# Kernel optimization log

Hardware: AMD Instinct MI355X
Metric: run time of the kernel (lower is better)

Reference implementation:

```python
import jax, jax.numpy as jnp
import numpy as np

B, CIN, HID, HEADS, K, STRIDE, PAD, W = 8, 256, 256, 8, 31, 1, 15, 16384
HD = HID // HEADS  # head dim
DN = ('NCHW', 'OIHW', 'NCHW')


def setup_inputs() -> dict:
    key = jax.random.key(0)
    ks = jax.random.split(key, 6)
    std = 1.0 / np.sqrt(HD)
    return dict(
        x=jax.random.normal(ks[0], (B, CIN, 1, W), jnp.float32),
        query=(jax.random.normal(ks[1], (HID,), jnp.float32) * std),
        Wk=(jax.random.normal(ks[2], (CIN, HID), jnp.float32) * std),
        Wk_bias=jnp.zeros((HID,), jnp.float32),
        rpe=0.02 * jax.random.normal(ks[3], (HEADS, 1, 1, K), jnp.float32),
        to_v_w=(jax.random.normal(ks[4], (HID, CIN, 1, 1), jnp.float32) / np.sqrt(CIN)),
        to_v_b=jnp.zeros((HID,), jnp.float32),
        to_out_w=(jax.random.normal(ks[5], (HID, HID, 1, 1), jnp.float32) / np.sqrt(HID)),
        to_out_b=jnp.zeros((HID,), jnp.float32),
    )


def reference(x, query, Wk, Wk_bias, rpe, to_v_w, to_v_b, to_out_w, to_out_b):
    Bsz = x.shape[0]
    # shared learned query -> [B, heads, hd], normalized and scaled
    q = jnp.broadcast_to(query, (Bsz, HID)).reshape(Bsz, HEADS, HD)
    q = q / (jnp.linalg.norm(q, axis=-1, keepdims=True) + 1e-6)
    q = q / np.sqrt(HD)
    # fused QK: (q @ Wk^T) @ x  -> cost [B, heads, 1, W]
    Wk_r = Wk.reshape(CIN, HEADS, HD)
    qWk = jnp.einsum('bhd,Dhd->bDh', q, Wk_r)          # [B, CIN, heads]
    cost = jnp.einsum('bDhw,bDc->bchw', x, qWk)        # [B, heads, 1, W]
    qWk_b = jnp.einsum('hd,bhd->bh', Wk_bias.reshape(HEADS, HD), q)
    cost = cost + qWk_b[:, :, None, None]
    cost_exp = jnp.exp(cost)
    # v = 1x1 conv (to_v)
    v = jnp.einsum('bdhw,od->bohw', x, to_v_w.reshape(HID, CIN)) + to_v_b[None, :, None, None]
    # exp-weighted values, grouped windowed sums
    vc = (cost_exp[:, :, None] * v.reshape(Bsz, HEADS, HD, 1, W)).reshape(Bsz, HID, 1, W)
    rpe_exp = jnp.exp(rpe)                             # [heads, 1, 1, K]
    kern_v = jnp.repeat(rpe_exp, HD, axis=0)           # [HID, 1, 1, K] depthwise
    sum_v = jax.lax.conv_general_dilated(
        vc, kern_v, (1, STRIDE), ((0, 0), (PAD, PAD)),
        feature_group_count=HID, dimension_numbers=DN)
    sum_c = jax.lax.conv_general_dilated(
        cost_exp, rpe_exp, (1, STRIDE), ((0, 0), (PAD, PAD)),
        feature_group_count=HEADS, dimension_numbers=DN)
    Wo = sum_v.shape[-1]
    out = sum_v.reshape(Bsz, HEADS, HD, 1, Wo) / sum_c.reshape(Bsz, HEADS, 1, 1, Wo)
    out = out.reshape(Bsz, HID, 1, Wo)
    # to_out 1x1 conv
    out = jnp.einsum('bdhw,od->bohw', out, to_out_w.reshape(HID, HID)) + to_out_b[None, :, None, None]
    return out
```

## Files before the change

kernel.cpp:

```cpp
#include <hip/hip_runtime.h>
#include <hip/hip_bf16.h>
#include <math.h>

#define BATCH  8
#define NHEADS 8
#define KW     31
#define W      16384

#define WS_QWKB 2048
#define WS_RPE  2056
#define OFF_WVH 9216
#define OFF_WOH (OFF_WVH + 131072)
#define OFF_CE  (OFF_WOH + 131072)

typedef __attribute__((ext_vector_type(8))) short  short8;
typedef __attribute__((ext_vector_type(4))) float  f32x4;

__device__ __forceinline__ float f4c(const float4& v, int i) {
  switch (i) { case 0: return v.x; case 1: return v.y; case 2: return v.z; default: return v.w; }
}
__device__ __forceinline__ unsigned short f2bf(float f) {
  union { __hip_bfloat16 h; unsigned short u; } cv; cv.h = __float2bfloat16(f); return cv.u;
}
__device__ __forceinline__ float bf2f(unsigned short u) {
  union { __hip_bfloat16 h; unsigned short u; } cv; cv.u = u; return __bfloat162float(cv.h);
}

__global__ __launch_bounds__(256) void prep_kernel(
    const float* __restrict__ query, const float* __restrict__ Wk,
    const float* __restrict__ Wkb, const float* __restrict__ rpe,
    const float* __restrict__ Wv, const float* __restrict__ Wo,
    float* __restrict__ ws, unsigned short* __restrict__ WvH,
    unsigned short* __restrict__ WoH) {
  int t = threadIdx.x, bid = blockIdx.x;
  if (bid == 0) {
    __shared__ float q_l[256];
    float qv = query[t];
    float ss = qv * qv;
    #pragma unroll
    for (int m = 16; m >= 1; m >>= 1) ss += __shfl_xor(ss, m, 32);
    qv = qv / (sqrtf(ss) + 1e-6f) * 0.17677669529663687f;
    q_l[t] = qv;
    __syncthreads();
    const float* wr = Wk + (size_t)t * 256;
    #pragma unroll
    for (int h = 0; h < 8; ++h) {
      float s = 0.f;
      #pragma unroll
      for (int d = 0; d < 32; ++d) s = fmaf(q_l[h*32 + d], wr[h*32 + d], s);
      ws[t*8 + h] = s;
    }
    float pb = Wkb[t] * q_l[t];
    #pragma unroll
    for (int m = 16; m >= 1; m >>= 1) pb += __shfl_xor(pb, m, 32);
    if ((t & 31) == 0) ws[WS_QWKB + (t >> 5)] = pb;
    if (t < NHEADS * KW) ws[WS_RPE + t] = __expf(rpe[t]);
  } else {
    const float* src = (bid <= 4) ? Wv : Wo;
    unsigned short* dst = (bid <= 4) ? WvH : WoH;
    int seg = (bid - 1) & 3;
    int base4 = seg * 4096;
    #pragma unroll
    for (int it = 0; it < 16; ++it) {
      int i4 = base4 + t + 256 * it;
      float4 v = ((const float4*)src)[i4];
      ushort4 o;
      o.x = f2bf(v.x); o.y = f2bf(v.y); o.z = f2bf(v.z); o.w = f2bf(v.w);
      ((ushort4*)dst)[i4] = o;
    }
  }
}

__global__ __launch_bounds__(512, 4) void xv_kernel(
    const float* __restrict__ x, const float* __restrict__ wsf,
    const unsigned short* __restrict__ A,
    const float* __restrict__ bias,
    float* __restrict__ ceout, float* __restrict__ vcout, int b0) {
  __shared__ float xs[64 * 260];
  __shared__ float cbuf[4 * 576];
  __shared__ float ceL[512];
  __shared__ float biasL[256];

  int t = threadIdx.x;
  int bb = blockIdx.y, b = b0 + bb;
  int w0 = blockIdx.x * 64;
  if (t < 256) biasL[t] = bias[t];

  {
    int tt = t & 255, db2 = t >> 8;
    int rr = tt >> 4, c2 = tt & 15;
    #pragma unroll
    for (int dd = 0; dd < 2; ++dd) {
      int db = db2 * 2 + dd;
      float4 v0 = *(const float4*)(x + ((size_t)b*256 + db*64 + rr*4 + 0)*W + w0 + c2*4);
      float4 v1 = *(const float4*)(x + ((size_t)b*256 + db*64 + rr*4 + 1)*W + w0 + c2*4);
      float4 v2 = *(const float4*)(x + ((size_t)b*256 + db*64 + rr*4 + 2)*W + w0 + c2*4);
      float4 v3 = *(const float4*)(x + ((size_t)b*256 + db*64 + rr*4 + 3)*W + w0 + c2*4);
      #pragma unroll
      for (int i = 0; i < 4; ++i) {
        float4 tv = make_float4(f4c(v0,i), f4c(v1,i), f4c(v2,i), f4c(v3,i));
        *(float4*)&xs[(c2*4 + i)*260 + db*64 + rr*4] = tv;
      }
    }
  }
  __syncthreads();

  int w = t & 63, q = t >> 6;
  int qu = __builtin_amdgcn_readfirstlane(q);

  f32x4 xr[8];
  {
    const float* xrow = &xs[w*260 + qu*32];
    #pragma unroll
    for (int i = 0; i < 8; ++i) xr[i] = *(const f32x4*)(xrow + 4*i);
    float ca[8] = {0,0,0,0,0,0,0,0};
    const float* qkb = wsf + (size_t)qu*256;
    #pragma unroll
    for (int k4 = 0; k4 < 8; ++k4) {
      const float* qr = qkb + k4*32;
      #pragma unroll
      for (int e = 0; e < 4; ++e) {
        #pragma unroll
        for (int h = 0; h < 8; ++h)
          ca[h] = fmaf(xr[k4][e], qr[e*8 + h], ca[h]);
      }
    }
    if (q < 4) {
      #pragma unroll
      for (int h = 0; h < 8; ++h) cbuf[q*576 + w*9 + h] = ca[h];
    } else {
      #pragma unroll
      for (int h = 0; h < 8; ++h) { asm volatile("" :: "v"(ca[h])); }
    }
    __syncthreads();

    {
      unsigned short* hrow = (unsigned short*)xs + w*520 + qu*32;
      #pragma unroll
      for (int kc = 0; kc < 4; ++kc) {
        short8 hs, ls;
        #pragma unroll
        for (int e = 0; e < 4; ++e) {
          float a0 = xr[2*kc][e], a1 = xr[2*kc+1][e];
          unsigned short h0 = f2bf(a0), h1 = f2bf(a1);
          hs[e]   = (short)h0;  hs[e+4] = (short)h1;
          ls[e]   = (short)f2bf(a0 - bf2f(h0));
          ls[e+4] = (short)f2bf(a1 - bf2f(h1));
        }
        *(short8*)(hrow + 8*kc)       = hs;
        *(short8*)(hrow + 256 + 8*kc) = ls;
      }
    }
    float acc0;
    {
      int hR = t >> 6 & 7, wR = t & 63;
      acc0 = cbuf[0*576 + wR*9 + hR] + cbuf[1*576 + wR*9 + hR]
           + cbuf[2*576 + wR*9 + hR] + cbuf[3*576 + wR*9 + hR];
    }
    __syncthreads();
    if (q >= 4) {
      #pragma unroll
      for (int h = 0; h < 8; ++h) cbuf[(q-4)*576 + w*9 + h] = ca[h];
    }
    __syncthreads();

    {
      int hR = t >> 6 & 7, wR = t & 63;
      float sum = acc0 + cbuf[0*576 + wR*9 + hR] + cbuf[1*576 + wR*9 + hR]
                + cbuf[2*576 + wR*9 + hR] + cbuf[3*576 + wR*9 + hR]
                + wsf[WS_QWKB + hR];
      float ce = __expf(sum);
      ceL[hR*64 + wR] = ce;
      ceout[((size_t)bb*8 + hR)*W + w0 + wR] = ce;
    }
  }
  __syncthreads();

  int wid = t >> 6, quad = (t >> 4) & 3, m = t & 15;
  f32x4 acc[2][4];
  #pragma unroll
  for (int j = 0; j < 2; ++j)
    #pragma unroll
    for (int c = 0; c < 4; ++c) acc[j][c] = (f32x4){0.f, 0.f, 0.f, 0.f};

  const unsigned short* xsu = (const unsigned short*)xs;
  #pragma unroll
  for (int kk = 0; kk < 8; ++kk) {
    int ko = kk*32 + quad*8;
    short8 a0 = *(const short8*)(A + (size_t)(32*wid + m)*256 + ko);
    short8 a1 = *(const short8*)(A + (size_t)(32*wid + 16 + m)*256 + ko);
    #pragma unroll
    for (int c = 0; c < 4; ++c) {
      int rw = 16*c + m;
      short8 bh = *(const short8*)(xsu + rw*520 + ko);
      short8 bl = *(const short8*)(xsu + rw*520 + 256 + ko);
      acc[0][c] = __builtin_amdgcn_mfma_f32_16x16x32_bf16(a0, bh, acc[0][c], 0, 0, 0);
      acc[0][c] = __builtin_amdgcn_mfma_f32_16x16x32_bf16(a0, bl, acc[0][c], 0, 0, 0);
      acc[1][c] = __builtin_amdgcn_mfma_f32_16x16x32_bf16(a1, bh, acc[1][c], 0, 0, 0);
      acc[1][c] = __builtin_amdgcn_mfma_f32_16x16x32_bf16(a1, bl, acc[1][c], 0, 0, 0);
    }
  }
  __syncthreads();

  #pragma unroll
  for (int j = 0; j < 2; ++j) {
    int ob = 32*wid + 16*j + 4*quad;
    #pragma unroll
    for (int c = 0; c < 4; ++c) {
      int wc = 16*c + m;
      float ce = ceL[wid*64 + wc];
      f32x4 r;
      #pragma unroll
      for (int i = 0; i < 4; ++i) r[i] = (acc[j][c][i] + biasL[ob + i]) * ce;
      *(f32x4*)(xs + wc*260 + ob) = r;
    }
  }
  __syncthreads();
  {
    float* vg = vcout + ((size_t)bb*W + w0)*256;
    #pragma unroll
    for (int it = 0; it < 8; ++it) {
      int idx = t + 512*it;
      int row = idx >> 6, c4 = (idx & 63)*4;
      f32x4 v = *(const f32x4*)(xs + row*260 + c4);
      *(f32x4*)(vg + (size_t)idx*4) = v;
    }
  }
}

__global__ __launch_bounds__(512, 6) void cg_kernel(
    const float* __restrict__ vc, const float* __restrict__ costexp,
    const float* __restrict__ rpe_ws, const unsigned short* __restrict__ A,
    const float* __restrict__ bias, float* __restrict__ outp, int b0) {
  __shared__ __align__(16) float vcl[62 * 36];
  __shared__ __align__(16) unsigned short ubuf[2][32*264];
  __shared__ float cel[8 * 64];
  __shared__ float rcl[8 * 32];
  __shared__ float rpel[8 * 32];
  __shared__ float biasL[256];

  int t = threadIdx.x;
  int bb = blockIdx.y;
  int tx = blockIdx.x;
  int tile = ((tx & 7) << 6) | (tx >> 3);
  int w0 = tile * 32;

  if (t < 256) {
    biasL[t] = bias[t];
    int h = t >> 5, k = t & 31;
    rpel[t] = (k < KW) ? rpe_ws[h*KW + k] : 0.f;
  }
  {
    int h = t >> 6, c = t & 63;
    if (c < 62) {
      int gw = w0 - 15 + c;
      cel[h*64 + c] = (gw >= 0 && gw < W) ? costexp[((size_t)bb*8 + h)*W + gw] : 0.f;
    }
  }
  __syncthreads();
  if (t < 256) {
    int h = t >> 5, w = t & 31;
    float acc = 0.f;
    #pragma unroll
    for (int k = 0; k < KW; ++k) acc = fmaf(rpel[h*32 + k], cel[h*64 + w + k], acc);
    rcl[t] = 1.0f / acc;
  }

  int wv = t >> 4, p = t & 15;
  for (int q = 0; q < 8; ++q) {
    if (t < 496) {
      int r = t >> 3, c4 = (t & 7) * 4;
      int gw = w0 - 15 + r;
      float4 v = make_float4(0.f, 0.f, 0.f, 0.f);
      if (gw >= 0 && gw < W)
        v = *(const float4*)(vc + ((size_t)bb*W + gw)*256 + q*32 + c4);
      *(float4*)&vcl[r*36 + c4] = v;
    }
    __syncthreads();
    {
      float ax = 0.f, ay = 0.f;
      #pragma unroll
      for (int k = 0; k < KW; ++k) {
        float rpk = rpel[q*32 + k];
        float2 v = *(const float2*)&vcl[(wv + k)*36 + 2*p];
        ax = fmaf(rpk, v.x, ax);
        ay = fmaf(rpk, v.y, ay);
      }
      float rc = rcl[q*32 + wv];
      float ux = ax * rc, uy = ay * rc;
      unsigned short hx = f2bf(ux), hy = f2bf(uy);
      unsigned short lx = f2bf(ux - bf2f(hx)), ly = f2bf(uy - bf2f(hy));
      ushort2 hv; hv.x = hx; hv.y = hy;
      ushort2 lv; lv.x = lx; lv.y = ly;
      *(ushort2*)&ubuf[0][wv*264 + q*32 + 2*p] = hv;
      *(ushort2*)&ubuf[1][wv*264 + q*32 + 2*p] = lv;
    }
    __syncthreads();
  }

  int wid = t >> 6, quad = (t >> 4) & 3, m = t & 15;
  f32x4 acc[2][2];
  #pragma unroll
  for (int j = 0; j < 2; ++j)
    #pragma unroll
    for (int c = 0; c < 2; ++c) acc[j][c] = (f32x4){0.f, 0.f, 0.f, 0.f};

  #pragma unroll
  for (int pass = 0; pass < 2; ++pass) {
    const unsigned short* bsrc = ubuf[pass];
    #pragma unroll
    for (int kk = 0; kk < 8; ++kk) {
      int ko = kk*32 + quad*8;
      short8 a0 = *(const short8*)(A + (size_t)(32*wid + m)*256 + ko);
      short8 a1 = *(const short8*)(A + (size_t)(32*wid + 16 + m)*256 + ko);
      #pragma unroll
      for (int c = 0; c < 2; ++c) {
        short8 bv = *(const short8*)(bsrc + (16*c + m)*264 + ko);
        acc[0][c] = __builtin_amdgcn_mfma_f32_16x16x32_bf16(a0, bv, acc[0][c], 0, 0, 0);
        acc[1][c] = __builtin_amdgcn_mfma_f32_16x16x32_bf16(a1, bv, acc[1][c], 0, 0, 0);
      }
    }
  }
  __syncthreads();

  float* outs = (float*)ubuf;
  #pragma unroll
  for (int j = 0; j < 2; ++j) {
    int ob = 32*wid + 16*j + 4*quad;
    #pragma unroll
    for (int c = 0; c < 2; ++c) {
      int w = 16*c + m;
      #pragma unroll
      for (int i = 0; i < 4; ++i)
        outs[(ob + i)*32 + w] = acc[j][c][i] + biasL[ob + i];
    }
  }
  __syncthreads();
  {
    float* og = outp + (size_t)(b0 + bb)*256*W + w0;
    #pragma unroll
    for (int it = 0; it < 4; ++it) {
      int idx = t + 512*it;
      int o = idx >> 3, c4 = (idx & 7)*4;
      f32x4 v = *(const f32x4*)(outs + o*32 + c4);
      *(f32x4*)(og + (size_t)o*W + c4) = v;
    }
  }
}

extern "C" void kernel_launch(void* const* d_in, const int* in_sizes, int n_in,
                              void* d_out, int out_size, void* d_ws, size_t ws_size,
                              hipStream_t stream) {
  const float* x     = (const float*)d_in[0];
  const float* query = (const float*)d_in[1];
  const float* Wk    = (const float*)d_in[2];
  const float* Wkb   = (const float*)d_in[3];
  const float* rpe   = (const float*)d_in[4];
  const float* Wv    = (const float*)d_in[5];
  const float* tvb   = (const float*)d_in[6];
  const float* Wo    = (const float*)d_in[7];
  const float* tob   = (const float*)d_in[8];
  float* out = (float*)d_out;
  char* wsb  = (char*)d_ws;
  float* wsf = (float*)d_ws;

  unsigned short* WvH = (unsigned short*)(wsb + OFF_WVH);
  unsigned short* WoH = (unsigned short*)(wsb + OFF_WOH);

  const size_t per_b = (size_t)8*W*4 + (size_t)W*256*4;
  int NB = (int)((ws_size > OFF_CE) ? ((ws_size - OFF_CE) / per_b) : 1);
  if (NB > BATCH) NB = BATCH;
  if (NB < 1) NB = 1;

  float* ceB = (float*)(wsb + OFF_CE);
  float* vcB = (float*)(wsb + OFF_CE + (size_t)NB*8*W*4);

  prep_kernel<<<9, 256, 0, stream>>>(query, Wk, Wkb, rpe, Wv, Wo, wsf, WvH, WoH);

  for (int b0 = 0; b0 < BATCH; b0 += NB) {
    int nb = (BATCH - b0 < NB) ? (BATCH - b0) : NB;
    xv_kernel<<<dim3(256, nb), 512, 0, stream>>>(x, wsf, WvH, tvb, ceB, vcB, b0);
    cg_kernel<<<dim3(512, nb), 512, 0, stream>>>(vcB, ceB, wsf + WS_RPE, WoH, tob, out, b0);
  }
}
```

Before: 469.1 us.

## Enlarge per-thread work in xv and cg kernels, cut sync and reload passes

xv_kernel drops to 256 threads per block. Each wave now computes a 64x64 MFMA tile with four A fragments reused across four B fragments, and the cost reduction uses one cbuf pass instead of two staged ones. cg_kernel loads half the channels (128) per iteration instead of 32, so there are 2 outer iterations rather than 8. Each thread computes two adjacent output positions from shared vc loads and keeps rpe in registers, and the output staging reuses vcl so one barrier is removed. The aim is fewer barriers and less LDS traffic per FLOP, at the cost of higher register pressure and lower occupancy.

```diff
diff --git a/kernel.cpp b/kernel.cpp
--- a/kernel.cpp
+++ b/kernel.cpp
@@ -71,27 +71,25 @@
   }
 }
 
-__global__ __launch_bounds__(512, 4) void xv_kernel(
+__global__ __launch_bounds__(256, 2) void xv_kernel(
     const float* __restrict__ x, const float* __restrict__ wsf,
     const unsigned short* __restrict__ A,
     const float* __restrict__ bias,
     float* __restrict__ ceout, float* __restrict__ vcout, int b0) {
   __shared__ float xs[64 * 260];
-  __shared__ float cbuf[4 * 576];
+  __shared__ float cbuf[2048];
   __shared__ float ceL[512];
   __shared__ float biasL[256];
 
   int t = threadIdx.x;
   int bb = blockIdx.y, b = b0 + bb;
   int w0 = blockIdx.x * 64;
-  if (t < 256) biasL[t] = bias[t];
-
-  {
-    int tt = t & 255, db2 = t >> 8;
-    int rr = tt >> 4, c2 = tt & 15;
-    #pragma unroll
-    for (int dd = 0; dd < 2; ++dd) {
-      int db = db2 * 2 + dd;
+  biasL[t] = bias[t];
+
+  {
+    int rr = t >> 4, c2 = t & 15;
+    #pragma unroll
+    for (int db = 0; db < 4; ++db) {
       float4 v0 = *(const float4*)(x + ((size_t)b*256 + db*64 + rr*4 + 0)*W + w0 + c2*4);
       float4 v1 = *(const float4*)(x + ((size_t)b*256 + db*64 + rr*4 + 1)*W + w0 + c2*4);
       float4 v2 = *(const float4*)(x + ((size_t)b*256 + db*64 + rr*4 + 2)*W + w0 + c2*4);
@@ -108,78 +106,65 @@
   int w = t & 63, q = t >> 6;
   int qu = __builtin_amdgcn_readfirstlane(q);
 
-  f32x4 xr[8];
-  {
-    const float* xrow = &xs[w*260 + qu*32];
-    #pragma unroll
-    for (int i = 0; i < 8; ++i) xr[i] = *(const f32x4*)(xrow + 4*i);
+  f32x4 xr[16];
+  {
+    const float* xrow = &xs[w*260 + qu*64];
+    #pragma unroll
+    for (int i = 0; i < 16; ++i) xr[i] = *(const f32x4*)(xrow + 4*i);
     float ca[8] = {0,0,0,0,0,0,0,0};
-    const float* qkb = wsf + (size_t)qu*256;
-    #pragma unroll
-    for (int k4 = 0; k4 < 8; ++k4) {
-      const float* qr = qkb + k4*32;
+    const float* qkb = wsf + (size_t)qu*64*8;
+    #pragma unroll
+    for (int k8 = 0; k8 < 8; ++k8) {
+      const float* qr = qkb + 64*k8;
       #pragma unroll
       for (int e = 0; e < 4; ++e) {
         #pragma unroll
-        for (int h = 0; h < 8; ++h)
-          ca[h] = fmaf(xr[k4][e], qr[e*8 + h], ca[h]);
-      }
-    }
-    if (q < 4) {
-      #pragma unroll
-      for (int h = 0; h < 8; ++h) cbuf[q*576 + w*9 + h] = ca[h];
-    } else {
-      #pragma unroll
-      for (int h = 0; h < 8; ++h) { asm volatile("" :: "v"(ca[h])); }
-    }
-    __syncthreads();
-
-    {
-      unsigned short* hrow = (unsigned short*)xs + w*520 + qu*32;
-      #pragma unroll
-      for (int kc = 0; kc < 4; ++kc) {
-        short8 hs, ls;
-        #pragma unroll
-        for (int e = 0; e < 4; ++e) {
-          float a0 = xr[2*kc][e], a1 = xr[2*kc+1][e];
-          unsigned short h0 = f2bf(a0), h1 = f2bf(a1);
-          hs[e]   = (short)h0;  hs[e+4] = (short)h1;
-          ls[e]   = (short)f2bf(a0 - bf2f(h0));
-          ls[e+4] = (short)f2bf(a1 - bf2f(h1));
+        for (int h = 0; h < 8; ++h) {
+          ca[h] = fmaf(xr[2*k8][e],   qr[e*8 + h],     ca[h]);
+          ca[h] = fmaf(xr[2*k8+1][e], qr[(e+4)*8 + h], ca[h]);
         }
-        *(short8*)(hrow + 8*kc)       = hs;
-        *(short8*)(hrow + 256 + 8*kc) = ls;
-      }
-    }
-    float acc0;
-    {
-      int hR = t >> 6 & 7, wR = t & 63;
-      acc0 = cbuf[0*576 + wR*9 + hR] + cbuf[1*576 + wR*9 + hR]
-           + cbuf[2*576 + wR*9 + hR] + cbuf[3*576 + wR*9 + hR];
-    }
-    __syncthreads();
-    if (q >= 4) {
-      #pragma unroll
-      for (int h = 0; h < 8; ++h) cbuf[(q-4)*576 + w*9 + h] = ca[h];
-    }
-    __syncthreads();
-
-    {
-      int hR = t >> 6 & 7, wR = t & 63;
-      float sum = acc0 + cbuf[0*576 + wR*9 + hR] + cbuf[1*576 + wR*9 + hR]
-                + cbuf[2*576 + wR*9 + hR] + cbuf[3*576 + wR*9 + hR]
-                + wsf[WS_QWKB + hR];
-      float ce = __expf(sum);
-      ceL[hR*64 + wR] = ce;
-      ceout[((size_t)bb*8 + hR)*W + w0 + wR] = ce;
-    }
+      }
+    }
+    #pragma unroll
+    for (int h = 0; h < 8; ++h) cbuf[t*8 + h] = ca[h];
+  }
+  __syncthreads();
+
+  {
+    unsigned short* hrow = (unsigned short*)xs + w*520 + qu*64;
+    #pragma unroll
+    for (int k8 = 0; k8 < 8; ++k8) {
+      short8 hs, ls;
+      #pragma unroll
+      for (int e = 0; e < 4; ++e) {
+        float a0 = xr[2*k8][e], a1 = xr[2*k8+1][e];
+        unsigned short h0 = f2bf(a0), h1 = f2bf(a1);
+        hs[e]   = (short)h0;  hs[e+4] = (short)h1;
+        ls[e]   = (short)f2bf(a0 - bf2f(h0));
+        ls[e+4] = (short)f2bf(a1 - bf2f(h1));
+      }
+      *(short8*)(hrow + 8*k8)       = hs;
+      *(short8*)(hrow + 256 + 8*k8) = ls;
+    }
+  }
+  __syncthreads();
+
+  #pragma unroll
+  for (int s = 0; s < 2; ++s) {
+    int idx = t + 256*s;
+    int h = idx >> 6, ww = idx & 63;
+    float sum = cbuf[ww*8 + h] + cbuf[(64+ww)*8 + h] + cbuf[(128+ww)*8 + h]
+              + cbuf[(192+ww)*8 + h] + wsf[WS_QWKB + h];
+    float ce = __expf(sum);
+    ceL[h*64 + ww] = ce;
+    ceout[((size_t)bb*8 + h)*W + w0 + ww] = ce;
   }
   __syncthreads();
 
   int wid = t >> 6, quad = (t >> 4) & 3, m = t & 15;
-  f32x4 acc[2][4];
-  #pragma unroll
-  for (int j = 0; j < 2; ++j)
+  f32x4 acc[4][4];
+  #pragma unroll
+  for (int j = 0; j < 4; ++j)
     #pragma unroll
     for (int c = 0; c < 4; ++c) acc[j][c] = (f32x4){0.f, 0.f, 0.f, 0.f};
 
@@ -187,28 +172,34 @@
   #pragma unroll
   for (int kk = 0; kk < 8; ++kk) {
     int ko = kk*32 + quad*8;
-    short8 a0 = *(const short8*)(A + (size_t)(32*wid + m)*256 + ko);
-    short8 a1 = *(const short8*)(A + (size_t)(32*wid + 16 + m)*256 + ko);
+    short8 a[4], bh[4], bl[4];
+    #pragma unroll
+    for (int j = 0; j < 4; ++j)
+      a[j] = *(const short8*)(A + (size_t)(64*wid + 16*j + m)*256 + ko);
     #pragma unroll
     for (int c = 0; c < 4; ++c) {
       int rw = 16*c + m;
-      short8 bh = *(const short8*)(xsu + rw*520 + ko);
-      short8 bl = *(const short8*)(xsu + rw*520 + 256 + ko);
-      acc[0][c] = __builtin_amdgcn_mfma_f32_16x16x32_bf16(a0, bh, acc[0][c], 0, 0, 0);
-      acc[0][c] = __builtin_amdgcn_mfma_f32_16x16x32_bf16(a0, bl, acc[0][c], 0, 0, 0);
-      acc[1][c] = __builtin_amdgcn_mfma_f32_16x16x32_bf16(a1, bh, acc[1][c], 0, 0, 0);
-      acc[1][c] = __builtin_amdgcn_mfma_f32_16x16x32_bf16(a1, bl, acc[1][c], 0, 0, 0);
-    }
-  }
-  __syncthreads();
-
-  #pragma unroll
-  for (int j = 0; j < 2; ++j) {
-    int ob = 32*wid + 16*j + 4*quad;
+      bh[c] = *(const short8*)(xsu + rw*520 + ko);
+      bl[c] = *(const short8*)(xsu + rw*520 + 256 + ko);
+    }
+    #pragma unroll
+    for (int j = 0; j < 4; ++j)
+      #pragma unroll
+      for (int c = 0; c < 4; ++c) {
+        acc[j][c] = __builtin_amdgcn_mfma_f32_16x16x32_bf16(a[j], bh[c], acc[j][c], 0, 0, 0);
+        acc[j][c] = __builtin_amdgcn_mfma_f32_16x16x32_bf16(a[j], bl[c], acc[j][c], 0, 0, 0);
+      }
+  }
+  __syncthreads();
+
+  #pragma unroll
+  for (int j = 0; j < 4; ++j) {
+    int ob = 64*wid + 16*j + 4*quad;
+    int h = (64*wid + 16*j) >> 5;
     #pragma unroll
     for (int c = 0; c < 4; ++c) {
       int wc = 16*c + m;
-      float ce = ceL[wid*64 + wc];
+      float ce = ceL[h*64 + wc];
       f32x4 r;
       #pragma unroll
       for (int i = 0; i < 4; ++i) r[i] = (acc[j][c][i] + biasL[ob + i]) * ce;
@@ -219,8 +210,8 @@
   {
     float* vg = vcout + ((size_t)bb*W + w0)*256;
     #pragma unroll
-    for (int it = 0; it < 8; ++it) {
-      int idx = t + 512*it;
+    for (int it = 0; it < 16; ++it) {
+      int idx = t + 256*it;
       int row = idx >> 6, c4 = (idx & 63)*4;
       f32x4 v = *(const f32x4*)(xs + row*260 + c4);
       *(f32x4*)(vg + (size_t)idx*4) = v;
@@ -228,12 +219,12 @@
   }
 }
 
-__global__ __launch_bounds__(512, 6) void cg_kernel(
+__global__ __launch_bounds__(512, 4) void cg_kernel(
     const float* __restrict__ vc, const float* __restrict__ costexp,
     const float* __restrict__ rpe_ws, const unsigned short* __restrict__ A,
     const float* __restrict__ bias, float* __restrict__ outp, int b0) {
-  __shared__ __align__(16) float vcl[62 * 36];
-  __shared__ __align__(16) unsigned short ubuf[2][32*264];
+  __shared__ __align__(16) float vcl[63 * 132];
+  __shared__ __align__(16) unsigned short ubuf[32 * 528];
   __shared__ float cel[8 * 64];
   __shared__ float rcl[8 * 32];
   __shared__ float rpel[8 * 32];
@@ -266,34 +257,57 @@
     rcl[t] = 1.0f / acc;
   }
 
-  int wv = t >> 4, p = t & 15;
-  for (int q = 0; q < 8; ++q) {
-    if (t < 496) {
-      int r = t >> 3, c4 = (t & 7) * 4;
-      int gw = w0 - 15 + r;
-      float4 v = make_float4(0.f, 0.f, 0.f, 0.f);
-      if (gw >= 0 && gw < W)
-        v = *(const float4*)(vc + ((size_t)bb*W + gw)*256 + q*32 + c4);
-      *(float4*)&vcl[r*36 + c4] = v;
+  int g = t >> 5, p4 = t & 31;
+  for (int half = 0; half < 2; ++half) {
+    #pragma unroll
+    for (int it = 0; it < 4; ++it) {
+      int idx = t + 512*it;
+      int r = idx >> 5, fq = idx & 31;
+      if (r < 62) {
+        int gw = w0 - 15 + r;
+        float4 v = make_float4(0.f, 0.f, 0.f, 0.f);
+        if (gw >= 0 && gw < W)
+          v = *(const float4*)(vc + ((size_t)bb*W + gw)*256 + half*128 + fq*4);
+        *(float4*)&vcl[r*132 + fq*4] = v;
+      }
     }
     __syncthreads();
+
     {
-      float ax = 0.f, ay = 0.f;
-      #pragma unroll
-      for (int k = 0; k < KW; ++k) {
-        float rpk = rpel[q*32 + k];
-        float2 v = *(const float2*)&vcl[(wv + k)*36 + 2*p];
-        ax = fmaf(rpk, v.x, ax);
-        ay = fmaf(rpk, v.y, ay);
-      }
-      float rc = rcl[q*32 + wv];
-      float ux = ax * rc, uy = ay * rc;
-      unsigned short hx = f2bf(ux), hy = f2bf(uy);
-      unsigned short lx = f2bf(ux - bf2f(hx)), ly = f2bf(uy - bf2f(hy));
-      ushort2 hv; hv.x = hx; hv.y = hy;
-      ushort2 lv; lv.x = lx; lv.y = ly;
-      *(ushort2*)&ubuf[0][wv*264 + q*32 + 2*p] = hv;
-      *(ushort2*)&ubuf[1][wv*264 + q*32 + 2*p] = lv;
+      int h = 4*half + (p4 >> 3);
+      float rp[KW];
+      #pragma unroll
+      for (int k = 0; k < KW; ++k) rp[k] = rpel[h*32 + k];
+
+      f32x4 a0 = (f32x4){0.f,0.f,0.f,0.f}, a1 = (f32x4){0.f,0.f,0.f,0.f};
+      #pragma unroll
+      for (int s = 0; s < 32; ++s) {
+        f32x4 v = *(const f32x4*)&vcl[(2*g + s)*132 + 4*p4];
+        if (s < KW) {
+          #pragma unroll
+          for (int e = 0; e < 4; ++e) a0[e] = fmaf(rp[s], v[e], a0[e]);
+        }
+        if (s >= 1) {
+          #pragma unroll
+          for (int e = 0; e < 4; ++e) a1[e] = fmaf(rp[s-1], v[e], a1[e]);
+        }
+      }
+      float rc0 = rcl[h*32 + 2*g], rc1 = rcl[h*32 + 2*g + 1];
+      ushort4 h0v, l0v, h1v, l1v;
+      #pragma unroll
+      for (int e = 0; e < 4; ++e) {
+        float u0 = a0[e] * rc0, u1 = a1[e] * rc1;
+        unsigned short hh0 = f2bf(u0), hh1 = f2bf(u1);
+        ((unsigned short*)&h0v)[e] = hh0;
+        ((unsigned short*)&l0v)[e] = f2bf(u0 - bf2f(hh0));
+        ((unsigned short*)&h1v)[e] = hh1;
+        ((unsigned short*)&l1v)[e] = f2bf(u1 - bf2f(hh1));
+      }
+      int cbase = half*128 + 4*p4;
+      *(ushort4*)&ubuf[(2*g    )*528 + cbase]       = h0v;
+      *(ushort4*)&ubuf[(2*g    )*528 + 256 + cbase] = l0v;
+      *(ushort4*)&ubuf[(2*g + 1)*528 + cbase]       = h1v;
+      *(ushort4*)&ubuf[(2*g + 1)*528 + 256 + cbase] = l1v;
     }
     __syncthreads();
   }
@@ -307,7 +321,6 @@
 
   #pragma unroll
   for (int pass = 0; pass < 2; ++pass) {
-    const unsigned short* bsrc = ubuf[pass];
     #pragma unroll
     for (int kk = 0; kk < 8; ++kk) {
       int ko = kk*32 + quad*8;
@@ -315,15 +328,14 @@
       short8 a1 = *(const short8*)(A + (size_t)(32*wid + 16 + m)*256 + ko);
       #pragma unroll
       for (int c = 0; c < 2; ++c) {
-        short8 bv = *(const short8*)(bsrc + (16*c + m)*264 + ko);
+        short8 bv = *(const short8*)(ubuf + (16*c + m)*528 + pass*256 + ko);
         acc[0][c] = __builtin_amdgcn_mfma_f32_16x16x32_bf16(a0, bv, acc[0][c], 0, 0, 0);
         acc[1][c] = __builtin_amdgcn_mfma_f32_16x16x32_bf16(a1, bv, acc[1][c], 0, 0, 0);
       }
     }
   }
-  __syncthreads();
-
-  float* outs = (float*)ubuf;
+
+  float* outs = (float*)vcl;
   #pragma unroll
   for (int j = 0; j < 2; ++j) {
     int ob = 32*wid + 16*j + 4*quad;
@@ -379,7 +391,7 @@
 
   for (int b0 = 0; b0 < BATCH; b0 += NB) {
     int nb = (BATCH - b0 < NB) ? (BATCH - b0) : NB;
-    xv_kernel<<<dim3(256, nb), 512, 0, stream>>>(x, wsf, WvH, tvb, ceB, vcB, b0);
+    xv_kernel<<<dim3(256, nb), 256, 0, stream>>>(x, wsf, WvH, tvb, ceB, vcB, b0);
     cg_kernel<<<dim3(512, nb), 512, 0, stream>>>(vcB, ceB, wsf + WS_RPE, WoH, tob, out, b0);
   }
 }
```

Result: faster. 419.5 us (-10.6%).

## Fuse value projection, windowed sum and output projection into one kernel with halo recompute

Applied to the files above, without the earlier changes.

Replaces the two-kernel pipeline (xv_kernel writing exp-cost and exp-weighted values to workspace, then cg_kernel reading them back) with a single 1024-thread kernel per 32-wide output tile. Each block loads a 64-wide x window including the halo, recomputes cost and the to_v projection for the halo columns, does the 31-tap windowed sums in registers, and applies the to_out MFMA. This removes the large round trip of the intermediate values through global memory and the per-batch launch loop. The cost is about double the value-projection MFMA work from halo recompute, plus larger blocks and a higher LDS footprint, which may reduce occupancy.

```diff
diff --git a/kernel.cpp b/kernel.cpp
--- a/kernel.cpp
+++ b/kernel.cpp
@@ -11,7 +11,6 @@
 #define WS_RPE  2056
 #define OFF_WVH 9216
 #define OFF_WOH (OFF_WVH + 131072)
-#define OFF_CE  (OFF_WOH + 131072)
 
 typedef __attribute__((ext_vector_type(8))) short  short8;
 typedef __attribute__((ext_vector_type(4))) float  f32x4;
@@ -71,276 +70,225 @@
   }
 }
 
-__global__ __launch_bounds__(512, 4) void xv_kernel(
+__global__ __launch_bounds__(1024, 4) void fused_kernel(
     const float* __restrict__ x, const float* __restrict__ wsf,
-    const unsigned short* __restrict__ A,
-    const float* __restrict__ bias,
-    float* __restrict__ ceout, float* __restrict__ vcout, int b0) {
-  __shared__ float xs[64 * 260];
-  __shared__ float cbuf[4 * 576];
+    const unsigned short* __restrict__ Av,
+    const unsigned short* __restrict__ Ao,
+    const float* __restrict__ biasv, const float* __restrict__ biaso,
+    float* __restrict__ outp) {
+  __shared__ __align__(16) float xs[64 * 260];
+  __shared__ __align__(16) float rgB[9216];
   __shared__ float ceL[512];
-  __shared__ float biasL[256];
+  __shared__ float rcl[256];
+  __shared__ float rpel[256];
+  __shared__ float bvL[256];
+  __shared__ float boL[256];
 
   int t = threadIdx.x;
-  int bb = blockIdx.y, b = b0 + bb;
-  int w0 = blockIdx.x * 64;
-  if (t < 256) biasL[t] = bias[t];
-
-  {
-    int tt = t & 255, db2 = t >> 8;
-    int rr = tt >> 4, c2 = tt & 15;
-    #pragma unroll
-    for (int dd = 0; dd < 2; ++dd) {
-      int db = db2 * 2 + dd;
-      float4 v0 = *(const float4*)(x + ((size_t)b*256 + db*64 + rr*4 + 0)*W + w0 + c2*4);
-      float4 v1 = *(const float4*)(x + ((size_t)b*256 + db*64 + rr*4 + 1)*W + w0 + c2*4);
-      float4 v2 = *(const float4*)(x + ((size_t)b*256 + db*64 + rr*4 + 2)*W + w0 + c2*4);
-      float4 v3 = *(const float4*)(x + ((size_t)b*256 + db*64 + rr*4 + 3)*W + w0 + c2*4);
-      #pragma unroll
-      for (int i = 0; i < 4; ++i) {
-        float4 tv = make_float4(f4c(v0,i), f4c(v1,i), f4c(v2,i), f4c(v3,i));
-        *(float4*)&xs[(c2*4 + i)*260 + db*64 + rr*4] = tv;
-      }
-    }
-  }
-  __syncthreads();
-
-  int w = t & 63, q = t >> 6;
-  int qu = __builtin_amdgcn_readfirstlane(q);
-
-  f32x4 xr[8];
-  {
-    const float* xrow = &xs[w*260 + qu*32];
-    #pragma unroll
-    for (int i = 0; i < 8; ++i) xr[i] = *(const f32x4*)(xrow + 4*i);
-    float ca[8] = {0,0,0,0,0,0,0,0};
-    const float* qkb = wsf + (size_t)qu*256;
-    #pragma unroll
-    for (int k4 = 0; k4 < 8; ++k4) {
-      const float* qr = qkb + k4*32;
-      #pragma unroll
-      for (int e = 0; e < 4; ++e) {
-        #pragma unroll
-        for (int h = 0; h < 8; ++h)
-          ca[h] = fmaf(xr[k4][e], qr[e*8 + h], ca[h]);
-      }
-    }
-    if (q < 4) {
-      #pragma unroll
-      for (int h = 0; h < 8; ++h) cbuf[q*576 + w*9 + h] = ca[h];
-    } else {
-      #pragma unroll
-      for (int h = 0; h < 8; ++h) { asm volatile("" :: "v"(ca[h])); }
-    }
-    __syncthreads();
-
-    {
-      unsigned short* hrow = (unsigned short*)xs + w*520 + qu*32;
-      #pragma unroll
-      for (int kc = 0; kc < 4; ++kc) {
-        short8 hs, ls;
-        #pragma unroll
-        for (int e = 0; e < 4; ++e) {
-          float a0 = xr[2*kc][e], a1 = xr[2*kc+1][e];
-          unsigned short h0 = f2bf(a0), h1 = f2bf(a1);
-          hs[e]   = (short)h0;  hs[e+4] = (short)h1;
-          ls[e]   = (short)f2bf(a0 - bf2f(h0));
-          ls[e+4] = (short)f2bf(a1 - bf2f(h1));
-        }
-        *(short8*)(hrow + 8*kc)       = hs;
-        *(short8*)(hrow + 256 + 8*kc) = ls;
-      }
-    }
-    float acc0;
-    {
-      int hR = t >> 6 & 7, wR = t & 63;
-      acc0 = cbuf[0*576 + wR*9 + hR] + cbuf[1*576 + wR*9 + hR]
-           + cbuf[2*576 + wR*9 + hR] + cbuf[3*576 + wR*9 + hR];
-    }
-    __syncthreads();
-    if (q >= 4) {
-      #pragma unroll
-      for (int h = 0; h < 8; ++h) cbuf[(q-4)*576 + w*9 + h] = ca[h];
-    }
-    __syncthreads();
-
-    {
-      int hR = t >> 6 & 7, wR = t & 63;
-      float sum = acc0 + cbuf[0*576 + wR*9 + hR] + cbuf[1*576 + wR*9 + hR]
-                + cbuf[2*576 + wR*9 + hR] + cbuf[3*576 + wR*9 + hR]
-                + wsf[WS_QWKB + hR];
-      float ce = __expf(sum);
-      ceL[hR*64 + wR] = ce;
-      ceout[((size_t)bb*8 + hR)*W + w0 + wR] = ce;
-    }
-  }
-  __syncthreads();
-
-  int wid = t >> 6, quad = (t >> 4) & 3, m = t & 15;
-  f32x4 acc[2][4];
-  #pragma unroll
-  for (int j = 0; j < 2; ++j)
-    #pragma unroll
-    for (int c = 0; c < 4; ++c) acc[j][c] = (f32x4){0.f, 0.f, 0.f, 0.f};
-
-  const unsigned short* xsu = (const unsigned short*)xs;
-  #pragma unroll
-  for (int kk = 0; kk < 8; ++kk) {
-    int ko = kk*32 + quad*8;
-    short8 a0 = *(const short8*)(A + (size_t)(32*wid + m)*256 + ko);
-    short8 a1 = *(const short8*)(A + (size_t)(32*wid + 16 + m)*256 + ko);
-    #pragma unroll
-    for (int c = 0; c < 4; ++c) {
-      int rw = 16*c + m;
-      short8 bh = *(const short8*)(xsu + rw*520 + ko);
-      short8 bl = *(const short8*)(xsu + rw*520 + 256 + ko);
-      acc[0][c] = __builtin_amdgcn_mfma_f32_16x16x32_bf16(a0, bh, acc[0][c], 0, 0, 0);
-      acc[0][c] = __builtin_amdgcn_mfma_f32_16x16x32_bf16(a0, bl, acc[0][c], 0, 0, 0);
-      acc[1][c] = __builtin_amdgcn_mfma_f32_16x16x32_bf16(a1, bh, acc[1][c], 0, 0, 0);
-      acc[1][c] = __builtin_amdgcn_mfma_f32_16x16x32_bf16(a1, bl, acc[1][c], 0, 0, 0);
-    }
-  }
-  __syncthreads();
-
-  #pragma unroll
-  for (int j = 0; j < 2; ++j) {
-    int ob = 32*wid + 16*j + 4*quad;
-    #pragma unroll
-    for (int c = 0; c < 4; ++c) {
-      int wc = 16*c + m;
-      float ce = ceL[wid*64 + wc];
-      f32x4 r;
-      #pragma unroll
-      for (int i = 0; i < 4; ++i) r[i] = (acc[j][c][i] + biasL[ob + i]) * ce;
-      *(f32x4*)(xs + wc*260 + ob) = r;
-    }
-  }
-  __syncthreads();
-  {
-    float* vg = vcout + ((size_t)bb*W + w0)*256;
-    #pragma unroll
-    for (int it = 0; it < 8; ++it) {
-      int idx = t + 512*it;
-      int row = idx >> 6, c4 = (idx & 63)*4;
-      f32x4 v = *(const f32x4*)(xs + row*260 + c4);
-      *(f32x4*)(vg + (size_t)idx*4) = v;
-    }
-  }
-}
-
-__global__ __launch_bounds__(512, 6) void cg_kernel(
-    const float* __restrict__ vc, const float* __restrict__ costexp,
-    const float* __restrict__ rpe_ws, const unsigned short* __restrict__ A,
-    const float* __restrict__ bias, float* __restrict__ outp, int b0) {
-  __shared__ __align__(16) float vcl[62 * 36];
-  __shared__ __align__(16) unsigned short ubuf[2][32*264];
-  __shared__ float cel[8 * 64];
-  __shared__ float rcl[8 * 32];
-  __shared__ float rpel[8 * 32];
-  __shared__ float biasL[256];
-
-  int t = threadIdx.x;
-  int bb = blockIdx.y;
+  int b = blockIdx.y;
   int tx = blockIdx.x;
   int tile = ((tx & 7) << 6) | (tx >> 3);
   int w0 = tile * 32;
 
   if (t < 256) {
-    biasL[t] = bias[t];
+    bvL[t] = biasv[t];
+    boL[t] = biaso[t];
     int h = t >> 5, k = t & 31;
-    rpel[t] = (k < KW) ? rpe_ws[h*KW + k] : 0.f;
-  }
-  {
-    int h = t >> 6, c = t & 63;
-    if (c < 62) {
-      int gw = w0 - 15 + c;
-      cel[h*64 + c] = (gw >= 0 && gw < W) ? costexp[((size_t)bb*8 + h)*W + gw] : 0.f;
-    }
-  }
-  __syncthreads();
+    rpel[t] = (k < KW) ? wsf[WS_RPE + h*KW + k] : 0.f;
+  }
+
+  {
+    int tt = t & 255, db = t >> 8;
+    int rr = tt >> 4, c2 = tt & 15;
+    int gwb = w0 - 16 + c2*4;
+    const float* xb = x + ((size_t)b*256 + db*64 + rr*4)*W + gwb;
+    float4 v0, v1, v2, v3;
+    if (gwb >= 0 && gwb + 3 < W) {
+      v0 = *(const float4*)(xb);
+      v1 = *(const float4*)(xb + W);
+      v2 = *(const float4*)(xb + 2*(size_t)W);
+      v3 = *(const float4*)(xb + 3*(size_t)W);
+    } else {
+      v0 = v1 = v2 = v3 = make_float4(0.f, 0.f, 0.f, 0.f);
+    }
+    #pragma unroll
+    for (int i = 0; i < 4; ++i) {
+      float4 tv = make_float4(f4c(v0,i), f4c(v1,i), f4c(v2,i), f4c(v3,i));
+      *(float4*)&xs[(c2*4 + i)*260 + db*64 + rr*4] = tv;
+    }
+  }
+  __syncthreads();
+
+  int w = t & 63, q = t >> 6;
+  int qu = __builtin_amdgcn_readfirstlane(q);
+
+  f32x4 xr[4];
+  {
+    const float* xrow = &xs[w*260 + qu*16];
+    #pragma unroll
+    for (int i = 0; i < 4; ++i) xr[i] = *(const f32x4*)(xrow + 4*i);
+    float ca[8] = {0,0,0,0,0,0,0,0};
+    const float* qr = wsf + (size_t)qu*128;
+    #pragma unroll
+    for (int k4 = 0; k4 < 4; ++k4)
+      #pragma unroll
+      for (int e = 0; e < 4; ++e)
+        #pragma unroll
+        for (int h = 0; h < 8; ++h)
+          ca[h] = fmaf(xr[k4][e], qr[(k4*4 + e)*8 + h], ca[h]);
+    #pragma unroll
+    for (int h = 0; h < 8; ++h) rgB[t*9 + h] = ca[h];
+  }
+  __syncthreads();
+
+  {
+    unsigned short* hrow = (unsigned short*)xs + w*520 + qu*16;
+    #pragma unroll
+    for (int kc = 0; kc < 2; ++kc) {
+      short8 hs, ls;
+      #pragma unroll
+      for (int e = 0; e < 4; ++e) {
+        float a0 = xr[2*kc][e], a1 = xr[2*kc+1][e];
+        unsigned short h0 = f2bf(a0), h1 = f2bf(a1);
+        hs[e]   = (short)h0;  hs[e+4] = (short)h1;
+        ls[e]   = (short)f2bf(a0 - bf2f(h0));
+        ls[e+4] = (short)f2bf(a1 - bf2f(h1));
+      }
+      *(short8*)(hrow + 8*kc)       = hs;
+      *(short8*)(hrow + 256 + 8*kc) = ls;
+    }
+  }
+  if (t < 512) {
+    int h = t >> 6, s = t & 63;
+    float sum = wsf[WS_QWKB + h];
+    #pragma unroll
+    for (int q2 = 0; q2 < 16; ++q2) sum += rgB[(q2*64 + s)*9 + h];
+    int gw = w0 - 16 + s;
+    ceL[h*64 + s] = (gw >= 0 && gw < W) ? __expf(sum) : 0.f;
+  }
+  __syncthreads();
+
   if (t < 256) {
-    int h = t >> 5, w = t & 31;
+    int h = t >> 5, ow = t & 31;
     float acc = 0.f;
     #pragma unroll
-    for (int k = 0; k < KW; ++k) acc = fmaf(rpel[h*32 + k], cel[h*64 + w + k], acc);
+    for (int k = 0; k < KW; ++k) acc = fmaf(rpel[h*32 + k], ceL[h*64 + ow + 1 + k], acc);
     rcl[t] = 1.0f / acc;
   }
 
-  int wv = t >> 4, p = t & 15;
-  for (int q = 0; q < 8; ++q) {
-    if (t < 496) {
-      int r = t >> 3, c4 = (t & 7) * 4;
-      int gw = w0 - 15 + r;
-      float4 v = make_float4(0.f, 0.f, 0.f, 0.f);
-      if (gw >= 0 && gw < W)
-        v = *(const float4*)(vc + ((size_t)bb*W + gw)*256 + q*32 + c4);
-      *(float4*)&vcl[r*36 + c4] = v;
-    }
-    __syncthreads();
-    {
-      float ax = 0.f, ay = 0.f;
-      #pragma unroll
-      for (int k = 0; k < KW; ++k) {
-        float rpk = rpel[q*32 + k];
-        float2 v = *(const float2*)&vcl[(wv + k)*36 + 2*p];
-        ax = fmaf(rpk, v.x, ax);
-        ay = fmaf(rpk, v.y, ay);
-      }
-      float rc = rcl[q*32 + wv];
-      float ux = ax * rc, uy = ay * rc;
-      unsigned short hx = f2bf(ux), hy = f2bf(uy);
-      unsigned short lx = f2bf(ux - bf2f(hx)), ly = f2bf(uy - bf2f(hy));
-      ushort2 hv; hv.x = hx; hv.y = hy;
-      ushort2 lv; lv.x = lx; lv.y = ly;
-      *(ushort2*)&ubuf[0][wv*264 + q*32 + 2*p] = hv;
-      *(ushort2*)&ubuf[1][wv*264 + q*32 + 2*p] = lv;
-    }
-    __syncthreads();
-  }
-
   int wid = t >> 6, quad = (t >> 4) & 3, m = t & 15;
-  f32x4 acc[2][2];
+  f32x4 acc1[4];
   #pragma unroll
-  for (int j = 0; j < 2; ++j)
-    #pragma unroll
-    for (int c = 0; c < 2; ++c) acc[j][c] = (f32x4){0.f, 0.f, 0.f, 0.f};
-
-  #pragma unroll
-  for (int pass = 0; pass < 2; ++pass) {
-    const unsigned short* bsrc = ubuf[pass];
+  for (int c = 0; c < 4; ++c) acc1[c] = (f32x4){0.f, 0.f, 0.f, 0.f};
+  {
+    const unsigned short* xsu = (const unsigned short*)xs;
     #pragma unroll
     for (int kk = 0; kk < 8; ++kk) {
       int ko = kk*32 + quad*8;
-      short8 a0 = *(const short8*)(A + (size_t)(32*wid + m)*256 + ko);
-      short8 a1 = *(const short8*)(A + (size_t)(32*wid + 16 + m)*256 + ko);
-      #pragma unroll
-      for (int c = 0; c < 2; ++c) {
-        short8 bv = *(const short8*)(bsrc + (16*c + m)*264 + ko);
-        acc[0][c] = __builtin_amdgcn_mfma_f32_16x16x32_bf16(a0, bv, acc[0][c], 0, 0, 0);
-        acc[1][c] = __builtin_amdgcn_mfma_f32_16x16x32_bf16(a1, bv, acc[1][c], 0, 0, 0);
-      }
-    }
-  }
-  __syncthreads();
-
-  float* outs = (float*)ubuf;
-  #pragma unroll
-  for (int j = 0; j < 2; ++j) {
-    int ob = 32*wid + 16*j + 4*quad;
+      short8 a = *(const short8*)(Av + (size_t)(16*wid + m)*256 + ko);
+      #pragma unroll
+      for (int c = 0; c < 4; ++c) {
+        short8 bh = *(const short8*)(xsu + (16*c + m)*520 + ko);
+        short8 bl = *(const short8*)(xsu + (16*c + m)*520 + 256 + ko);
+        acc1[c] = __builtin_amdgcn_mfma_f32_16x16x32_bf16(a, bh, acc1[c], 0, 0, 0);
+        acc1[c] = __builtin_amdgcn_mfma_f32_16x16x32_bf16(a, bl, acc1[c], 0, 0, 0);
+      }
+    }
+  }
+  __syncthreads();
+
+  {
+    int h = wid >> 1;
+    int ob = 16*wid + 4*quad;
+    #pragma unroll
+    for (int c = 0; c < 4; ++c) {
+      int s = 16*c + m;
+      float ce = ceL[h*64 + s];
+      f32x4 r;
+      #pragma unroll
+      for (int i = 0; i < 4; ++i) r[i] = (acc1[c][i] + bvL[ob + i]) * ce;
+      *(f32x4*)(xs + s*260 + ob) = r;
+    }
+  }
+  __syncthreads();
+
+  if (t < 512) {
+    int g = t >> 6, pc = t & 63;
+    int h = pc >> 3;
+    float rp[KW];
+    #pragma unroll
+    for (int k = 0; k < KW; ++k) rp[k] = rpel[h*32 + k];
+    f32x4 ac[4];
+    #pragma unroll
+    for (int j = 0; j < 4; ++j) ac[j] = (f32x4){0.f, 0.f, 0.f, 0.f};
+    #pragma unroll
+    for (int s = 0; s < 34; ++s) {
+      f32x4 v = *(const f32x4*)(xs + (4*g + 1 + s)*260 + 4*pc);
+      #pragma unroll
+      for (int j = 0; j < 4; ++j) {
+        int k = s - j;
+        if (k >= 0 && k < KW) {
+          #pragma unroll
+          for (int e = 0; e < 4; ++e) ac[j][e] = fmaf(rp[k], v[e], ac[j][e]);
+        }
+      }
+    }
+    unsigned short* ubuf = (unsigned short*)rgB;
+    #pragma unroll
+    for (int j = 0; j < 4; ++j) {
+      int ow = 4*g + j;
+      float rc = rcl[h*32 + ow];
+      ushort4 hv, lv;
+      #pragma unroll
+      for (int e = 0; e < 4; ++e) {
+        float u = ac[j][e] * rc;
+        unsigned short hh = f2bf(u);
+        ((unsigned short*)&hv)[e] = hh;
+        ((unsigned short*)&lv)[e] = f2bf(u - bf2f(hh));
+      }
+      *(ushort4*)&ubuf[ow*528 + 4*pc]       = hv;
+      *(ushort4*)&ubuf[ow*528 + 256 + 4*pc] = lv;
+    }
+  }
+  __syncthreads();
+
+  f32x4 acc2[2];
+  acc2[0] = (f32x4){0.f, 0.f, 0.f, 0.f};
+  acc2[1] = (f32x4){0.f, 0.f, 0.f, 0.f};
+  {
+    const unsigned short* ubuf = (const unsigned short*)rgB;
+    #pragma unroll
+    for (int pass = 0; pass < 2; ++pass) {
+      #pragma unroll
+      for (int kk = 0; kk < 8; ++kk) {
+        int ko = kk*32 + quad*8;
+        short8 a = *(const short8*)(Ao + (size_t)(16*wid + m)*256 + ko);
+        #pragma unroll
+        for (int c = 0; c < 2; ++c) {
+          short8 bv = *(const short8*)(ubuf + (16*c + m)*528 + pass*256 + ko);
+          acc2[c] = __builtin_amdgcn_mfma_f32_16x16x32_bf16(a, bv, acc2[c], 0, 0, 0);
+        }
+      }
+    }
+  }
+  {
+    float* outs = xs;
+    int ob = 16*wid + 4*quad;
     #pragma unroll
     for (int c = 0; c < 2; ++c) {
-      int w = 16*c + m;
+      int ww = 16*c + m;
       #pragma unroll
       for (int i = 0; i < 4; ++i)
-        outs[(ob + i)*32 + w] = acc[j][c][i] + biasL[ob + i];
-    }
-  }
-  __syncthreads();
-  {
-    float* og = outp + (size_t)(b0 + bb)*256*W + w0;
-    #pragma unroll
-    for (int it = 0; it < 4; ++it) {
-      int idx = t + 512*it;
+        outs[(ob + i)*32 + ww] = acc2[c][i] + boL[ob + i];
+    }
+  }
+  __syncthreads();
+  {
+    const float* outs = xs;
+    float* og = outp + (size_t)b*256*W + w0;
+    #pragma unroll
+    for (int it = 0; it < 2; ++it) {
+      int idx = t + 1024*it;
       int o = idx >> 3, c4 = (idx & 7)*4;
       f32x4 v = *(const f32x4*)(outs + o*32 + c4);
       *(f32x4*)(og + (size_t)o*W + c4) = v;
@@ -363,23 +311,11 @@
   float* out = (float*)d_out;
   char* wsb  = (char*)d_ws;
   float* wsf = (float*)d_ws;
+  (void)in_sizes; (void)n_in; (void)out_size; (void)ws_size;
 
   unsigned short* WvH = (unsigned short*)(wsb + OFF_WVH);
   unsigned short* WoH = (unsigned short*)(wsb + OFF_WOH);
 
-  const size_t per_b = (size_t)8*W*4 + (size_t)W*256*4;
-  int NB = (int)((ws_size > OFF_CE) ? ((ws_size - OFF_CE) / per_b) : 1);
-  if (NB > BATCH) NB = BATCH;
-  if (NB < 1) NB = 1;
-
-  float* ceB = (float*)(wsb + OFF_CE);
-  float* vcB = (float*)(wsb + OFF_CE + (size_t)NB*8*W*4);
-
   prep_kernel<<<9, 256, 0, stream>>>(query, Wk, Wkb, rpe, Wv, Wo, wsf, WvH, WoH);
-
-  for (int b0 = 0; b0 < BATCH; b0 += NB) {
-    int nb = (BATCH - b0 < NB) ? (BATCH - b0) : NB;
-    xv_kernel<<<dim3(256, nb), 512, 0, stream>>>(x, wsf, WvH, tvb, ceB, vcB, b0);
-    cg_kernel<<<dim3(512, nb), 512, 0, stream>>>(vcB, ceB, wsf + WS_RPE, WoH, tob, out, b0);
-  }
-}
+  fused_kernel<<<dim3(512, BATCH), 1024, 0, stream>>>(x, wsf, WvH, WoH, tvb, tob, out);
+}
```

Measured after the change: 563.0 us. +20.0%, slower.
